# Optimization experiments

Hardware: AMD Instinct MI355X
Metric: run time of the kernel (lower is better)

The kernel has to match this reference:

```python
import jax, jax.numpy as jnp
import numpy as np

B, N, D, H, W, C = 4, 1, 48, 32, 88, 64
NX, NY, NZ = 200, 200, 1  # bev grid from (bound_hi - bound_lo) / resolution


def setup_inputs() -> dict:
    key = jax.random.key(0)
    k1, k2, k3 = jax.random.split(key, 3)
    x = jax.random.normal(k1, (B, N, D, H, W, C), jnp.float32)
    u = jax.random.uniform(k2, (B, N, D, H, W, 3), jnp.float32)
    lo = jnp.array([-50.0, -50.0, -10.0], jnp.float32)
    hi = jnp.array([50.0, 50.0, 10.0], jnp.float32)
    geom_feats = lo + u * (hi - lo)  # ego-frame xyz of each frustum point
    semantic_mask = jax.random.uniform(k3, (B * N, 2, H, W), jnp.float32)
    dx = jnp.array([0.5, 0.5, 20.0], jnp.float32)          # voxel size
    bx = jnp.array([-49.75, -49.75, 0.0], jnp.float32)     # voxel-center origin
    return {"x": x, "geom_feats": geom_feats, "semantic_mask": semantic_mask,
            "dx": dx, "bx": bx}


def reference(x, geom_feats, semantic_mask, dx, bx):
    Bs, Ns, Ds, Hs, Ws, Cs = x.shape
    Nprime = Bs * Ns * Ds * Hs * Ws
    xf = x.reshape(Nprime, Cs)
    # torch .long() truncates toward zero; jnp astype(int) does the same
    g = ((geom_feats - (bx - dx / 2.0)) / dx).reshape(Nprime, 3).astype(jnp.int32)
    batch_ix = jnp.repeat(jnp.arange(Bs, dtype=jnp.int32), Nprime // Bs)
    kept = ((g[:, 0] >= 0) & (g[:, 0] < NX) &
            (g[:, 1] >= 0) & (g[:, 1] < NY) &
            (g[:, 2] >= 0) & (g[:, 2] < NZ))
    # semantic_mask[:,1] > 0.5 broadcast over depth bins
    sm = (semantic_mask[:, 1] > 0.5)[:, None, None, :, :]        # [B*N,1,1,H,W]
    sm = jnp.broadcast_to(sm, (Bs * Ns, 1, Ds, Hs, Ws)).reshape(-1)
    kept = kept & sm
    # Sum features per voxel directly into the dense grid (equivalent to the
    # sort + cumsum-trick VoxelsSumming followed by index_put, since each voxel
    # receives the sum of all its points exactly once).
    nvox = Bs * NZ * NX * NY
    idx = ((batch_ix * NZ + g[:, 2]) * NX + g[:, 0]) * NY + g[:, 1]
    idx = jnp.where(kept, idx, nvox)                 # dropped points -> dummy slot
    vals = jnp.where(kept[:, None], xf, jnp.zeros((), x.dtype))
    grid = jnp.zeros((nvox + 1, Cs), x.dtype).at[idx].add(vals)[:nvox]
    final = grid.reshape(Bs, NZ, NX, NY, Cs)         # (B, nz, nx0, nx1, C)
    # torch: final (B,C,nz,nx,ny) -> cat(unbind(dim=2), 1) == z-major channel stack
    final = jnp.transpose(final, (0, 1, 4, 2, 3)).reshape(Bs, NZ * Cs, NX, NY)
    return final
```

## Files before the change

kernel.cpp:

```cpp
#include <hip/hip_runtime.h>

#define B_  4
#define N_  1
#define D_  48
#define H_  32
#define W_  88
#define C_  64
#define NX_ 200
#define NY_ 200
#define NZ_ 1
#define NPRIME (B_ * N_ * D_ * H_ * W_)
#define NXY    (NX_ * NY_)
#define NVOX   (B_ * NXY)

__global__ __launch_bounds__(256)
void hist_kernel(const float* __restrict__ geom,
                 const float* __restrict__ sem,
                 const float* __restrict__ dxp,
                 const float* __restrict__ bxp,
                 int* __restrict__ voxid,
                 int* __restrict__ counts)
{
    int p = blockIdx.x * 256 + threadIdx.x;
    int w = p % W_;
    int t = p / W_;
    int h = t % H_;
    t /= H_;
    int b = t / D_;

    int v = -1;
    float sm = sem[(b * 2 + 1) * (H_ * W_) + h * W_ + w];
    if (sm > 0.5f) {
        float gxf = (geom[(size_t)p * 3 + 0] - (bxp[0] - dxp[0] * 0.5f)) / dxp[0];
        float gyf = (geom[(size_t)p * 3 + 1] - (bxp[1] - dxp[1] * 0.5f)) / dxp[1];
        float gzf = (geom[(size_t)p * 3 + 2] - (bxp[2] - dxp[2] * 0.5f)) / dxp[2];
        int gx = (int)gxf, gy = (int)gyf, gz = (int)gzf;
        if (gx >= 0 && gx < NX_ && gy >= 0 && gy < NY_ &&
            gz >= 0 && gz < NZ_) {
            v = b * NXY + gx * NY_ + gy;
            atomicAdd(&counts[v], 1);
        }
    }
    voxid[p] = v;
}

__global__ __launch_bounds__(256)
void scan1_kernel(const int* __restrict__ counts,
                  int* __restrict__ base,
                  int* __restrict__ partials)
{
    __shared__ int s[256];
    int t = threadIdx.x;
    int i = blockIdx.x * 256 + t;
    int c = counts[i];
    s[t] = c;
    __syncthreads();
    for (int off = 1; off < 256; off <<= 1) {
        int add = (t >= off) ? s[t - off] : 0;
        __syncthreads();
        s[t] += add;
        __syncthreads();
    }
    base[i] = s[t] - c;
    if (t == 255) partials[blockIdx.x] = s[255];
}

__global__ __launch_bounds__(1024)
void scan2_kernel(int* __restrict__ partials, int* __restrict__ base)
{
    __shared__ int s[1024];
    int t = threadIdx.x;
    s[t] = (t < 625) ? partials[t] : 0;
    __syncthreads();
    for (int off = 1; off < 1024; off <<= 1) {
        int add = (t >= off) ? s[t - off] : 0;
        __syncthreads();
        s[t] += add;
        __syncthreads();
    }
    if (t < 625) partials[t] = s[t];
    if (t == 624) base[NVOX] = s[624];
}

__global__ __launch_bounds__(256)
void scan3_kernel(int* __restrict__ base,
                  const int* __restrict__ partials,
                  int* __restrict__ cursor)
{
    int blk = blockIdx.x;
    int i = blk * 256 + threadIdx.x;
    int off = (blk > 0) ? partials[blk - 1] : 0;
    int bv = base[i] + off;
    base[i] = bv;
    cursor[i] = bv;
}

__global__ __launch_bounds__(256)
void fill_kernel(const int* __restrict__ voxid,
                 int* __restrict__ cursor,
                 int* __restrict__ plist)
{
    int p = blockIdx.x * 256 + threadIdx.x;
    int v = voxid[p];
    if (v >= 0) {
        int slot = atomicAdd(&cursor[v], 1);
        plist[slot] = p;
    }
}

__global__ __launch_bounds__(256)
void gather_kernel(const float* __restrict__ x,
                   const int* __restrict__ base,
                   const int* __restrict__ plist,
                   float* __restrict__ out)
{
    __shared__ float tile[64][65];
    int blk = blockIdx.x;
    int t    = threadIdx.x;
    int wave = t >> 6;
    int lane = t & 63;
    int g    = lane >> 4;
    int s    = lane & 15;
    int vbase = blk * 64;
    int b   = vbase / NXY;
    int xy0 = vbase % NXY;
    int v0 = vbase + wave * 16;

    int j0[17];
    #pragma unroll
    for (int i = 0; i < 17; ++i) j0[i] = base[v0 + i];

    int rmax = 0;
    #pragma unroll
    for (int i = 0; i < 16; ++i) rmax = max(rmax, j0[i + 1] - j0[i]);

    int jg[4], cg[4];
    #pragma unroll
    for (int k = 0; k < 4; ++k) {
        int a0 = j0[4 * k + 0], a1 = j0[4 * k + 1], a2 = j0[4 * k + 2];
        int a3 = j0[4 * k + 3], a4 = j0[4 * k + 4];
        int lo = (g & 2) ? ((g & 1) ? a3 : a2) : ((g & 1) ? a1 : a0);
        int hi = (g & 2) ? ((g & 1) ? a4 : a3) : ((g & 1) ? a2 : a1);
        jg[k] = lo;
        cg[k] = hi - lo;
    }

    float4 acc[4];
    #pragma unroll
    for (int k = 0; k < 4; ++k) acc[k] = make_float4(0.f, 0.f, 0.f, 0.f);

    for (int r = 0; r < rmax; ++r) {
        int e[4];
        #pragma unroll
        for (int k = 0; k < 4; ++k) {
            int idx = jg[k] + r;
            idx = min(idx, NPRIME - 1);
            e[k] = plist[idx];
        }
        #pragma unroll
        for (int k = 0; k < 4; ++k) {
            e[k] = (r < cg[k]) ? e[k] : 0;
            e[k] = min(max(e[k], 0), NPRIME - 1);
        }
        float4 val[4];
        #pragma unroll
        for (int k = 0; k < 4; ++k)
            val[k] = *(const float4*)(x + (size_t)e[k] * C_ + s * 4);
        #pragma unroll
        for (int k = 0; k < 4; ++k) {
            if (r < cg[k]) {
                acc[k].x += val[k].x; acc[k].y += val[k].y;
                acc[k].z += val[k].z; acc[k].w += val[k].w;
            }
        }
    }

    #pragma unroll
    for (int k = 0; k < 4; ++k) {
        int row = wave * 16 + 4 * k + g;
        tile[row][4 * s + 0] = acc[k].x;
        tile[row][4 * s + 1] = acc[k].y;
        tile[row][4 * s + 2] = acc[k].z;
        tile[row][4 * s + 3] = acc[k].w;
    }
    __syncthreads();

    int col = t & 63;
    int rg  = t >> 6;
    float* dst = out + (size_t)b * C_ * NXY + xy0;
    #pragma unroll
    for (int it = 0; it < 16; ++it) {
        int ch = it * 4 + rg;
        dst[(size_t)ch * NXY + col] = tile[col][ch];
    }
}

__global__ __launch_bounds__(256)
void scatter_direct(const float* __restrict__ x,
                    const float* __restrict__ geom,
                    const float* __restrict__ sem,
                    const float* __restrict__ dxp,
                    const float* __restrict__ bxp,
                    float* __restrict__ out)
{
    int gid = blockIdx.x * 256 + threadIdx.x;
    int p = gid >> 6;
    int c = gid & 63;
    if (p >= NPRIME) return;
    int w = p % W_;
    int t = p / W_;
    int h = t % H_;
    t /= H_;
    int b = t / D_;
    float sm = sem[(b * 2 + 1) * (H_ * W_) + h * W_ + w];
    if (!(sm > 0.5f)) return;
    float gxf = (geom[(size_t)p * 3 + 0] - (bxp[0] - dxp[0] * 0.5f)) / dxp[0];
    float gyf = (geom[(size_t)p * 3 + 1] - (bxp[1] - dxp[1] * 0.5f)) / dxp[1];
    float gzf = (geom[(size_t)p * 3 + 2] - (bxp[2] - dxp[2] * 0.5f)) / dxp[2];
    int gx = (int)gxf, gy = (int)gyf, gz = (int)gzf;
    if (gx < 0 || gx >= NX_ || gy < 0 || gy >= NY_ ||
        gz < 0 || gz >= NZ_) return;
    float val = x[(size_t)p * C_ + c];
    atomicAdd(&out[(((size_t)b * C_ + c) * NX_ + gx) * NY_ + gy], val);
}

extern "C" void kernel_launch(void* const* d_in, const int* in_sizes, int n_in,
                              void* d_out, int out_size, void* d_ws, size_t ws_size,
                              hipStream_t stream)
{
    const float* x    = (const float*)d_in[0];
    const float* geom = (const float*)d_in[1];
    const float* sem  = (const float*)d_in[2];
    const float* dxp  = (const float*)d_in[3];
    const float* bxp  = (const float*)d_in[4];
    float* out = (float*)d_out;

    char* wsb = (char*)d_ws;
    const size_t MB = 1024 * 1024;
    int* counts   = (int*)(wsb + 0 * MB);
    int* base     = (int*)(wsb + 1 * MB);
    int* cursor   = (int*)(wsb + 2 * MB);
    int* partials = (int*)(wsb + 3 * MB);
    int* voxid    = (int*)(wsb + 4 * MB);
    int* plist    = (int*)(wsb + 7 * MB);
    const size_t wsNeed = 10 * MB;

    if (ws_size >= wsNeed) {
        hipMemsetAsync(counts, 0, (size_t)NVOX * sizeof(int), stream);
        hist_kernel<<<NPRIME / 256, 256, 0, stream>>>(geom, sem, dxp, bxp,
                                                      voxid, counts);
        scan1_kernel<<<NVOX / 256, 256, 0, stream>>>(counts, base, partials);
        scan2_kernel<<<1, 1024, 0, stream>>>(partials, base);
        scan3_kernel<<<NVOX / 256, 256, 0, stream>>>(base, partials, cursor);
        fill_kernel<<<NPRIME / 256, 256, 0, stream>>>(voxid, cursor, plist);
        gather_kernel<<<NVOX / 64, 256, 0, stream>>>(x, base, plist, out);
    } else {
        hipMemsetAsync(out, 0, (size_t)B_ * C_ * NXY * sizeof(float), stream);
        int nBlocks = (NPRIME * 64 + 255) / 256;
        scatter_direct<<<nBlocks, 256, 0, stream>>>(x, geom, sem, dxp, bxp, out);
    }
}
```

Before: 251.0 us.

## Replace counting-sort pipeline with fixed-capacity per-voxel buckets plus overflow list

The histogram, three-pass prefix scan and fill kernels are replaced by a single kernel that atomically claims a slot in a fixed 16-entry bucket per voxel, spilling extra points to a global overflow list. The gather kernel reads bucket entries directly and then handles overflow points with per-channel atomics. This removes four kernel launches and the scan and fill passes over the point array. In exchange it needs a much larger bucket workspace and every gather block scans the whole overflow list, with atomics on output it has already written.

```diff
diff --git a/kernel.cpp b/kernel.cpp
--- a/kernel.cpp
+++ b/kernel.cpp
@@ -12,106 +12,51 @@
 #define NPRIME (B_ * N_ * D_ * H_ * W_)
 #define NXY    (NX_ * NY_)
 #define NVOX   (B_ * NXY)
+#define CAP    16
+#define OVFMAX 32768
 
 __global__ __launch_bounds__(256)
-void hist_kernel(const float* __restrict__ geom,
+void bucket_fill(const float* __restrict__ geom,
                  const float* __restrict__ sem,
                  const float* __restrict__ dxp,
                  const float* __restrict__ bxp,
-                 int* __restrict__ voxid,
-                 int* __restrict__ counts)
+                 int* __restrict__ counts,
+                 int* __restrict__ ovfcnt,
+                 int* __restrict__ ovfbuf,
+                 int* __restrict__ bucket)
 {
     int p = blockIdx.x * 256 + threadIdx.x;
     int w = p % W_;
     int t = p / W_;
     int h = t % H_;
-    t /= H_;
-    int b = t / D_;
-
-    int v = -1;
+    int b = (t / H_) / D_;
+
     float sm = sem[(b * 2 + 1) * (H_ * W_) + h * W_ + w];
-    if (sm > 0.5f) {
-        float gxf = (geom[(size_t)p * 3 + 0] - (bxp[0] - dxp[0] * 0.5f)) / dxp[0];
-        float gyf = (geom[(size_t)p * 3 + 1] - (bxp[1] - dxp[1] * 0.5f)) / dxp[1];
-        float gzf = (geom[(size_t)p * 3 + 2] - (bxp[2] - dxp[2] * 0.5f)) / dxp[2];
-        int gx = (int)gxf, gy = (int)gyf, gz = (int)gzf;
-        if (gx >= 0 && gx < NX_ && gy >= 0 && gy < NY_ &&
-            gz >= 0 && gz < NZ_) {
-            v = b * NXY + gx * NY_ + gy;
-            atomicAdd(&counts[v], 1);
-        }
-    }
-    voxid[p] = v;
+    if (!(sm > 0.5f)) return;
+
+    float gxf = (geom[(size_t)p * 3 + 0] - (bxp[0] - dxp[0] * 0.5f)) / dxp[0];
+    float gyf = (geom[(size_t)p * 3 + 1] - (bxp[1] - dxp[1] * 0.5f)) / dxp[1];
+    float gzf = (geom[(size_t)p * 3 + 2] - (bxp[2] - dxp[2] * 0.5f)) / dxp[2];
+    int gx = (int)gxf, gy = (int)gyf, gz = (int)gzf;
+    if (gx < 0 || gx >= NX_ || gy < 0 || gy >= NY_ ||
+        gz < 0 || gz >= NZ_) return;
+
+    int v = b * NXY + gx * NY_ + gy;
+    int slot = atomicAdd(&counts[v], 1);
+    if (slot < CAP) {
+        bucket[v * CAP + slot] = p;
+    } else {
+        int o = atomicAdd(ovfcnt, 1);
+        if (o < OVFMAX) { ovfbuf[2 * o] = p; ovfbuf[2 * o + 1] = v; }
+    }
 }
 
 __global__ __launch_bounds__(256)
-void scan1_kernel(const int* __restrict__ counts,
-                  int* __restrict__ base,
-                  int* __restrict__ partials)
-{
-    __shared__ int s[256];
-    int t = threadIdx.x;
-    int i = blockIdx.x * 256 + t;
-    int c = counts[i];
-    s[t] = c;
-    __syncthreads();
-    for (int off = 1; off < 256; off <<= 1) {
-        int add = (t >= off) ? s[t - off] : 0;
-        __syncthreads();
-        s[t] += add;
-        __syncthreads();
-    }
-    base[i] = s[t] - c;
-    if (t == 255) partials[blockIdx.x] = s[255];
-}
-
-__global__ __launch_bounds__(1024)
-void scan2_kernel(int* __restrict__ partials, int* __restrict__ base)
-{
-    __shared__ int s[1024];
-    int t = threadIdx.x;
-    s[t] = (t < 625) ? partials[t] : 0;
-    __syncthreads();
-    for (int off = 1; off < 1024; off <<= 1) {
-        int add = (t >= off) ? s[t - off] : 0;
-        __syncthreads();
-        s[t] += add;
-        __syncthreads();
-    }
-    if (t < 625) partials[t] = s[t];
-    if (t == 624) base[NVOX] = s[624];
-}
-
-__global__ __launch_bounds__(256)
-void scan3_kernel(int* __restrict__ base,
-                  const int* __restrict__ partials,
-                  int* __restrict__ cursor)
-{
-    int blk = blockIdx.x;
-    int i = blk * 256 + threadIdx.x;
-    int off = (blk > 0) ? partials[blk - 1] : 0;
-    int bv = base[i] + off;
-    base[i] = bv;
-    cursor[i] = bv;
-}
-
-__global__ __launch_bounds__(256)
-void fill_kernel(const int* __restrict__ voxid,
-                 int* __restrict__ cursor,
-                 int* __restrict__ plist)
-{
-    int p = blockIdx.x * 256 + threadIdx.x;
-    int v = voxid[p];
-    if (v >= 0) {
-        int slot = atomicAdd(&cursor[v], 1);
-        plist[slot] = p;
-    }
-}
-
-__global__ __launch_bounds__(256)
-void gather_kernel(const float* __restrict__ x,
-                   const int* __restrict__ base,
-                   const int* __restrict__ plist,
+void bucket_gather(const float* __restrict__ x,
+                   const int* __restrict__ counts,
+                   const int* __restrict__ bucket,
+                   const int* __restrict__ ovfcnt,
+                   const int* __restrict__ ovfbuf,
                    float* __restrict__ out)
 {
     __shared__ float tile[64][65];
@@ -126,23 +71,22 @@
     int xy0 = vbase % NXY;
     int v0 = vbase + wave * 16;
 
-    int j0[17];
-    #pragma unroll
-    for (int i = 0; i < 17; ++i) j0[i] = base[v0 + i];
+    int cnt[16];
+    #pragma unroll
+    for (int i = 0; i < 16; ++i) cnt[i] = min(counts[v0 + i], CAP);
 
     int rmax = 0;
     #pragma unroll
-    for (int i = 0; i < 16; ++i) rmax = max(rmax, j0[i + 1] - j0[i]);
-
-    int jg[4], cg[4];
+    for (int i = 0; i < 16; ++i) rmax = max(rmax, cnt[i]);
+
+    int cg[4], jg[4];
     #pragma unroll
     for (int k = 0; k < 4; ++k) {
-        int a0 = j0[4 * k + 0], a1 = j0[4 * k + 1], a2 = j0[4 * k + 2];
-        int a3 = j0[4 * k + 3], a4 = j0[4 * k + 4];
-        int lo = (g & 2) ? ((g & 1) ? a3 : a2) : ((g & 1) ? a1 : a0);
-        int hi = (g & 2) ? ((g & 1) ? a4 : a3) : ((g & 1) ? a2 : a1);
-        jg[k] = lo;
-        cg[k] = hi - lo;
+        int c0 = cnt[4 * k + 0], c1 = cnt[4 * k + 1];
+        int c2 = cnt[4 * k + 2], c3 = cnt[4 * k + 3];
+        int cc = (g & 2) ? ((g & 1) ? c3 : c2) : ((g & 1) ? c1 : c0);
+        cg[k] = cc;
+        jg[k] = (v0 + 4 * k + g) * CAP;
     }
 
     float4 acc[4];
@@ -152,11 +96,8 @@
     for (int r = 0; r < rmax; ++r) {
         int e[4];
         #pragma unroll
-        for (int k = 0; k < 4; ++k) {
-            int idx = jg[k] + r;
-            idx = min(idx, NPRIME - 1);
-            e[k] = plist[idx];
-        }
+        for (int k = 0; k < 4; ++k)
+            e[k] = bucket[jg[k] + r];
         #pragma unroll
         for (int k = 0; k < 4; ++k) {
             e[k] = (r < cg[k]) ? e[k] : 0;
@@ -192,6 +133,23 @@
     for (int it = 0; it < 16; ++it) {
         int ch = it * 4 + rg;
         dst[(size_t)ch * NXY + col] = tile[col][ch];
+    }
+
+    int novf = min(ovfcnt[0], OVFMAX);
+    if (novf > 0) {
+        __syncthreads();
+        __threadfence();
+        for (int i = 0; i < novf; ++i) {
+            int pv = ovfbuf[2 * i + 1];
+            int c0 = pv - vbase;
+            if (c0 == t) {
+                int pp = min(max(ovfbuf[2 * i], 0), NPRIME - 1);
+                const float* xr = x + (size_t)pp * C_;
+                float* d2 = out + (size_t)b * C_ * NXY + xy0 + c0;
+                for (int ch = 0; ch < C_; ++ch)
+                    atomicAdd(&d2[(size_t)ch * NXY], xr[ch]);
+            }
+        }
     }
 }
 
@@ -237,23 +195,19 @@
 
     char* wsb = (char*)d_ws;
     const size_t MB = 1024 * 1024;
-    int* counts   = (int*)(wsb + 0 * MB);
-    int* base     = (int*)(wsb + 1 * MB);
-    int* cursor   = (int*)(wsb + 2 * MB);
-    int* partials = (int*)(wsb + 3 * MB);
-    int* voxid    = (int*)(wsb + 4 * MB);
-    int* plist    = (int*)(wsb + 7 * MB);
-    const size_t wsNeed = 10 * MB;
+    int* counts = (int*)(wsb + 0 * MB);
+    int* ovfcnt = counts + NVOX;
+    int* ovfbuf = (int*)(wsb + 1 * MB);
+    int* bucket = (int*)(wsb + 2 * MB);
+    const size_t wsNeed = 2 * MB + (size_t)NVOX * CAP * sizeof(int);
 
     if (ws_size >= wsNeed) {
-        hipMemsetAsync(counts, 0, (size_t)NVOX * sizeof(int), stream);
-        hist_kernel<<<NPRIME / 256, 256, 0, stream>>>(geom, sem, dxp, bxp,
-                                                      voxid, counts);
-        scan1_kernel<<<NVOX / 256, 256, 0, stream>>>(counts, base, partials);
-        scan2_kernel<<<1, 1024, 0, stream>>>(partials, base);
-        scan3_kernel<<<NVOX / 256, 256, 0, stream>>>(base, partials, cursor);
-        fill_kernel<<<NPRIME / 256, 256, 0, stream>>>(voxid, cursor, plist);
-        gather_kernel<<<NVOX / 64, 256, 0, stream>>>(x, base, plist, out);
+        hipMemsetAsync(counts, 0, ((size_t)NVOX + 16) * sizeof(int), stream);
+        bucket_fill<<<NPRIME / 256, 256, 0, stream>>>(geom, sem, dxp, bxp,
+                                                      counts, ovfcnt, ovfbuf,
+                                                      bucket);
+        bucket_gather<<<NVOX / 64, 256, 0, stream>>>(x, counts, bucket,
+                                                     ovfcnt, ovfbuf, out);
     } else {
         hipMemsetAsync(out, 0, (size_t)B_ * C_ * NXY * sizeof(float), stream);
         int nBlocks = (NPRIME * 64 + 255) / 256;
```

Measured after the change: 237.0 us. -5.6%, faster.
